# Optimization experiments

Hardware: AMD Instinct MI355X
Metric: run time of the kernel (lower is better)

Reference implementation:

```python
import jax, jax.numpy as jnp
import numpy as np

B, D, T, H = 1024, 128, 256, 64  # batch, input_dim, seq_len, hidden_dim


def _lstm_layer(x_proj, w_hh):
    """x_proj: [B, T, 4H] precomputed input projection (incl. both biases).
    Returns (all hidden states [B, T, H], final hidden [B, H])."""
    b = x_proj.shape[0]
    h0 = jnp.zeros((b, H), x_proj.dtype)
    c0 = jnp.zeros((b, H), x_proj.dtype)

    def step(carry, xt):
        h, c = carry
        gates = xt + h @ w_hh.T  # [B, 4H]; PyTorch gate order i, f, g, o
        i, f, g, o = jnp.split(gates, 4, axis=-1)
        i = jax.nn.sigmoid(i)
        f = jax.nn.sigmoid(f)
        g = jnp.tanh(g)
        o = jax.nn.sigmoid(o)
        c = f * c + i * g
        h = o * jnp.tanh(c)
        return (h, c), h

    (hT, _), ys = jax.lax.scan(step, (h0, c0), x_proj.transpose(1, 0, 2))
    return ys.transpose(1, 0, 2), hT


def setup_inputs() -> dict:
    key = jax.random.key(0)
    ks = jax.random.split(key, 11)
    s = 1.0 / np.sqrt(H)  # PyTorch LSTM init scale
    return {
        "x": jax.random.normal(ks[0], (B, D, T), jnp.float32),
        "w_ih0": jax.random.normal(ks[1], (4 * H, D), jnp.float32) * s,
        "w_hh0": jax.random.normal(ks[2], (4 * H, H), jnp.float32) * s,
        "b_ih0": jax.random.normal(ks[3], (4 * H,), jnp.float32) * s,
        "b_hh0": jax.random.normal(ks[4], (4 * H,), jnp.float32) * s,
        "w_ih1": jax.random.normal(ks[5], (4 * H, H), jnp.float32) * s,
        "w_hh1": jax.random.normal(ks[6], (4 * H, H), jnp.float32) * s,
        "b_ih1": jax.random.normal(ks[7], (4 * H,), jnp.float32) * s,
        "b_hh1": jax.random.normal(ks[8], (4 * H,), jnp.float32) * s,
        "w_fc": jax.random.normal(ks[9], (D, H), jnp.float32) * s,
        "b_fc": jax.random.normal(ks[10], (D,), jnp.float32) * s,
    }


def reference(x, w_ih0, w_hh0, b_ih0, b_hh0, w_ih1, w_hh1, b_ih1, b_hh1, w_fc, b_fc):
    # x: [B, input_dim, T] -> permute(0, 2, 1) -> [B, T, input_dim]
    xt = x.transpose(0, 2, 1)
    # Layer 0: precompute input projection for all timesteps (one big GEMM)
    xp0 = xt @ w_ih0.T + (b_ih0 + b_hh0)  # [B, T, 4H]
    ys0, _ = _lstm_layer(xp0, w_hh0)
    # Inter-layer dropout(p=0.3) is identity in eval/inference mode.
    xp1 = ys0 @ w_ih1.T + (b_ih1 + b_hh1)  # [B, T, 4H]
    _, hT = _lstm_layer(xp1, w_hh1)
    # Final-timestep linear head: lstm_out[:, -1, :] == final hidden state hT
    scores = hT @ w_fc.T + b_fc  # [B, input_dim]
    return scores
```

## Files before the change

### kernel.cpp

```cpp
#include <hip/hip_runtime.h>

#define PH  72
#define HSZ 1152
#define XRW 144
#define XSL 584

typedef float f32x4 __attribute__((ext_vector_type(4)));
typedef _Float16 f16x8 __attribute__((ext_vector_type(8)));

__device__ __forceinline__ float sigmoid_f(float x) {
    float e = __builtin_amdgcn_exp2f(-1.4426950408889634f * x);
    return __builtin_amdgcn_rcpf(1.0f + e);
}
__device__ __forceinline__ float tanh_f(float x) {
    float e = __builtin_amdgcn_exp2f(-2.8853900817779268f * x);
    return 2.0f * __builtin_amdgcn_rcpf(1.0f + e) - 1.0f;
}
__device__ __forceinline__ f16x8 load_frag16h(const float* wp, int n, int K, int k0) {
    const float* wf = wp + (size_t)n * K + k0;
    f16x8 h;
    #pragma unroll
    for (int j = 0; j < 8; ++j) h[j] = (_Float16)wf[j];
    return h;
}
__device__ __forceinline__ void load_frag16(const float* wp, int n, int K, int k0,
                                            f16x8& hi, f16x8& lo) {
    const float* wf = wp + (size_t)n * K + k0;
    #pragma unroll
    for (int j = 0; j < 8; ++j) {
        const float v = wf[j];
        const _Float16 h = (_Float16)v;
        hi[j] = h;
        lo[j] = (_Float16)(v - (float)h);
    }
}
__device__ __forceinline__ void gload16(const void* g, void* l) {
    __builtin_amdgcn_global_load_lds(
        (const __attribute__((address_space(1))) unsigned int*)g,
        (__attribute__((address_space(3))) unsigned int*)l, 16, 0, 0);
}

#define MFMA16(a, b, c) __builtin_amdgcn_mfma_f32_16x16x32_f16(a, b, c, 0, 0, 0)

__global__ __launch_bounds__(768, 3) void rec_fused(
    const float* __restrict__ x,
    const float* __restrict__ wih0, const float* __restrict__ whh0,
    const float* __restrict__ bih0, const float* __restrict__ bhh0,
    const float* __restrict__ wih1, const float* __restrict__ whh1,
    const float* __restrict__ bih1, const float* __restrict__ bhh1,
    const float* __restrict__ wfc,  const float* __restrict__ bfc,
    float* __restrict__ out)
{
    __shared__ float    xs32[4 * 2048];
    __shared__ _Float16 xh[32 * XSL];
    __shared__ float    xpl[4 * 1024];
    __shared__ _Float16 h0[2 * HSZ], h1[2 * HSZ];
    const int tid = threadIdx.x, lane = tid & 63, w = tid >> 6;
    const int l16 = lane & 15, quad = lane >> 4, k0 = quad * 8;
    const int wl = w & 3;
    const int role = w >> 2;
    const bool is1 = (role == 0), is0 = (role == 1), isP = (role == 2);
    const int bb  = blockIdx.x & 63;
    const int sub = blockIdx.x >> 6;

    const float* xrow = x + (size_t)(bb * 16 + wl * 4 + sub) * 128 * 256;

    f16x8 fA[4][2], fB[4][4];
    float gb[4] = {0.f, 0.f, 0.f, 0.f};
    #pragma unroll
    for (int g = 0; g < 4; ++g) {
        const int n = g * 64 + wl * 16 + l16;
        if (is1) {
            #pragma unroll
            for (int ks = 0; ks < 2; ++ks) {
                fA[g][ks] = load_frag16h(wih1, n, 64, ks * 32 + k0);
                load_frag16(whh1, n, 64, ks * 32 + k0, fB[g][ks], fB[g][2 + ks]);
            }
            gb[g] = bih1[n] + bhh1[n];
        } else if (is0) {
            #pragma unroll
            for (int ks = 0; ks < 2; ++ks)
                load_frag16(whh0, n, 64, ks * 32 + k0, fA[g][ks], fB[g][2 + ks]);
        } else {
            #pragma unroll
            for (int ks = 0; ks < 4; ++ks)
                fB[g][ks] = load_frag16h(wih0, n, 128, ks * 32 + k0);
            gb[g] = bih0[n] + bhh0[n];
        }
    }
    for (int i = tid; i < 2 * HSZ; i += 768) { h0[i] = (_Float16)0.f; h1[i] = (_Float16)0.f; }
    float c = 0.f;

    auto convert_rows = [&](int cc, int ib0, int nib) {
        const int sb = (cc & 1) * 16;
        const int tq = lane & 3;
        for (int ib = ib0; ib < ib0 + nib; ++ib) {
            const float4 v = *(const float4*)&xs32[wl * 2048 + ib * 256 + lane * 4];
            const int d = ib * 16 + (lane >> 2);
            const float vv[4] = {v.x, v.y, v.z, v.w};
            #pragma unroll
            for (int j = 0; j < 4; ++j)
                xh[(sb + tq * 4 + j) * XSL + wl * XRW + d] = (_Float16)vv[j];
        }
    };
    auto issue_chunk = [&](int cc) {
        #pragma unroll
        for (int ib = 0; ib < 8; ++ib)
            gload16(xrow + (size_t)(ib * 16 + (lane >> 2)) * 256 + cc * 16 + (lane & 3) * 4,
                    (char*)xs32 + wl * 8192 + ib * 1024);
    };
    auto compute_xp = [&](int tp) {
        const int fs = ((tp >> 4) & 1) * 16 + (tp & 15);
        f16x8 ax[4];
        #pragma unroll
        for (int ks = 0; ks < 4; ++ks)
            ax[ks] = *(const f16x8*)&xh[fs * XSL + (l16 >> 2) * XRW + ks * 32 + k0];
        f32x4 pa[4];
        #pragma unroll
        for (int g = 0; g < 4; ++g) pa[g] = (f32x4){gb[g], 0.f, 0.f, 0.f};
        #pragma unroll
        for (int g = 0; g < 4; ++g)
            #pragma unroll
            for (int ks = 0; ks < 4; ++ks)
                pa[g] = MFMA16(ax[ks], fB[g][ks], pa[g]);
        f32x4 o;
        o[0] = pa[0][0]; o[1] = pa[1][0]; o[2] = pa[2][0]; o[3] = pa[3][0];
        *(f32x4*)&xpl[(((tp & 3) * 4 + wl) * 64 + lane) * 4] = o;
    };

    if (isP) issue_chunk(0);
    __syncthreads();
    if (isP) { convert_rows(0, 0, 8); issue_chunk(1); }
    __syncthreads();
    if (isP) { compute_xp(0); compute_xp(1); }
    __syncthreads();
    if (is0) {
        const f32x4 xp4 = *(const f32x4*)&xpl[(wl * 64 + lane) * 4];
        const float gi = sigmoid_f(xp4[0]);
        const float gg = tanh_f(xp4[2]);
        const float go = sigmoid_f(xp4[3]);
        c = gi * gg;
        h0[(quad * 4) * PH + wl * 16 + l16] = (_Float16)(go * tanh_f(c));
    }
    __syncthreads();

    for (int t = 0; t < 255; ++t) {
        const int s0 = t & 1, s1 = s0 ^ 1;
        const int tn = t + 1;
        if (is1) {
            f16x8 ah[2], bh[2];
            #pragma unroll
            for (int ks = 0; ks < 2; ++ks) {
                ah[ks] = *(const f16x8*)&h0[s0 * HSZ + l16 * PH + ks * 32 + k0];
                bh[ks] = *(const f16x8*)&h1[s1 * HSZ + l16 * PH + ks * 32 + k0];
            }
            f32x4 accA[4], accB[4];
            #pragma unroll
            for (int g = 0; g < 4; ++g) {
                accA[g] = (f32x4){gb[g], 0.f, 0.f, 0.f};
                accB[g] = (f32x4){0.f, 0.f, 0.f, 0.f};
            }
            #pragma unroll
            for (int g = 0; g < 4; ++g)
                #pragma unroll
                for (int ks = 0; ks < 2; ++ks) {
                    accA[g] = MFMA16(ah[ks], fA[g][ks], accA[g]);
                    accA[g] = MFMA16(bh[ks], fB[g][ks], accA[g]);
                    accB[g] = MFMA16(bh[ks], fB[g][2 + ks], accB[g]);
                }
            const float gi = sigmoid_f(accA[0][0] + accB[0][0]);
            const float gf = sigmoid_f(accA[1][0] + accB[1][0]);
            const float gg = tanh_f(accA[2][0] + accB[2][0]);
            const float go = sigmoid_f(accA[3][0] + accB[3][0]);
            c = gf * c + gi * gg;
            h1[s0 * HSZ + (quad * 4) * PH + wl * 16 + l16] =
                (_Float16)(go * tanh_f(c));
        } else if (is0) {
            const f32x4 xp4 =
                *(const f32x4*)&xpl[(((tn & 3) * 4 + wl) * 64 + lane) * 4];
            f16x8 ah[2];
            #pragma unroll
            for (int ks = 0; ks < 2; ++ks)
                ah[ks] = *(const f16x8*)&h0[s0 * HSZ + l16 * PH + ks * 32 + k0];
            f32x4 accA[4], accB[4];
            #pragma unroll
            for (int g = 0; g < 4; ++g) {
                accA[g] = (f32x4){xp4[g], 0.f, 0.f, 0.f};
                accB[g] = (f32x4){0.f, 0.f, 0.f, 0.f};
            }
            #pragma unroll
            for (int g = 0; g < 4; ++g)
                #pragma unroll
                for (int ks = 0; ks < 2; ++ks) {
                    accA[g] = MFMA16(ah[ks], fA[g][ks], accA[g]);
                    accB[g] = MFMA16(ah[ks], fB[g][2 + ks], accB[g]);
                }
            const float gi = sigmoid_f(accA[0][0] + accB[0][0]);
            const float gf = sigmoid_f(accA[1][0] + accB[1][0]);
            const float gg = tanh_f(accA[2][0] + accB[2][0]);
            const float go = sigmoid_f(accA[3][0] + accB[3][0]);
            c = gf * c + gi * gg;
            h0[s1 * HSZ + (quad * 4) * PH + wl * 16 + l16] =
                (_Float16)(go * tanh_f(c));
        } else {
            if ((tn & 15) == 0 && tn < 240)
                issue_chunk((tn >> 4) + 1);
            const int m16 = tn & 15;
            if (m16 >= 8 && m16 < 12 && tn < 248)
                convert_rows((tn >> 4) + 1, (m16 - 8) * 2, 2);
            const int tp = t + 2;
            if (tp <= 255) compute_xp(tp);
        }
        __syncthreads();
    }

    if (is1) {
        f16x8 ah[2], bh[2];
        #pragma unroll
        for (int ks = 0; ks < 2; ++ks) {
            ah[ks] = *(const f16x8*)&h0[HSZ + l16 * PH + ks * 32 + k0];
            bh[ks] = *(const f16x8*)&h1[l16 * PH + ks * 32 + k0];
        }
        f32x4 accA[4], accB[4];
        #pragma unroll
        for (int g = 0; g < 4; ++g) {
            accA[g] = (f32x4){gb[g], 0.f, 0.f, 0.f};
            accB[g] = (f32x4){0.f, 0.f, 0.f, 0.f};
        }
        #pragma unroll
        for (int g = 0; g < 4; ++g)
            #pragma unroll
            for (int ks = 0; ks < 2; ++ks) {
                accA[g] = MFMA16(ah[ks], fA[g][ks], accA[g]);
                accA[g] = MFMA16(bh[ks], fB[g][ks], accA[g]);
                accB[g] = MFMA16(bh[ks], fB[g][2 + ks], accB[g]);
            }
        const float gi = sigmoid_f(accA[0][0] + accB[0][0]);
        const float gf = sigmoid_f(accA[1][0] + accB[1][0]);
        const float gg = tanh_f(accA[2][0] + accB[2][0]);
        const float go = sigmoid_f(accA[3][0] + accB[3][0]);
        c = gf * c + gi * gg;
        h1[HSZ + (quad * 4) * PH + wl * 16 + l16] = (_Float16)(go * tanh_f(c));
    }
    __syncthreads();

    if (tid < 512) {
        const int n   = tid & 127;
        const int sel = tid >> 7;
        float s = 0.f;
        for (int k = 0; k < 64; ++k)
            s += (float)h1[HSZ + (sel * 4) * PH + k] * wfc[n * 64 + k];
        out[(size_t)(bb * 16 + sel * 4 + sub) * 128 + n] = s + bfc[n];
    }
}

extern "C" void kernel_launch(void* const* d_in, const int* in_sizes, int n_in,
                              void* d_out, int out_size, void* d_ws, size_t ws_size,
                              hipStream_t stream) {
    const float* x     = (const float*)d_in[0];
    const float* wih0  = (const float*)d_in[1];
    const float* whh0  = (const float*)d_in[2];
    const float* bih0  = (const float*)d_in[3];
    const float* bhh0  = (const float*)d_in[4];
    const float* wih1  = (const float*)d_in[5];
    const float* whh1  = (const float*)d_in[6];
    const float* bih1  = (const float*)d_in[7];
    const float* bhh1  = (const float*)d_in[8];
    const float* wfc   = (const float*)d_in[9];
    const float* bfc   = (const float*)d_in[10];
    float* out = (float*)d_out;

    rec_fused<<<256, 768, 0, stream>>>(x, wih0, whh0, bih0, bhh0,
                                       wih1, whh1, bih1, bhh1, wfc, bfc, out);
}
```

Measured before the change: 365.8 us.

## Prefetch projection inputs into registers and prioritize recurrent waves

The layer-0 waves now load their input-projection vector one step ahead into a register. The projection waves preload their x fragments from LDS a step early and compute the projection three timesteps ahead instead of two. The recurrent waves raise their scheduling priority with s_setprio during the gate math. The goal is to take LDS load latency off the serial per-step critical path and let the recurrent waves win issue slots over the projection work, at the cost of extra live registers and a deeper ring of buffer slots.

```diff
diff --git a/kernel.cpp b/kernel.cpp
--- a/kernel.cpp
+++ b/kernel.cpp
@@ -90,6 +90,8 @@
     }
     for (int i = tid; i < 2 * HSZ; i += 768) { h0[i] = (_Float16)0.f; h1[i] = (_Float16)0.f; }
     float c = 0.f;
+    f32x4 xpr;
+    f16x8 axr[4];
 
     auto convert_rows = [&](int cc, int ib0, int nib) {
         const int sb = (cc & 1) * 16;
@@ -132,15 +134,21 @@
     __syncthreads();
     if (isP) { convert_rows(0, 0, 8); issue_chunk(1); }
     __syncthreads();
-    if (isP) { compute_xp(0); compute_xp(1); }
+    if (isP) { compute_xp(0); compute_xp(1); compute_xp(2); }
     __syncthreads();
     if (is0) {
-        const f32x4 xp4 = *(const f32x4*)&xpl[(wl * 64 + lane) * 4];
-        const float gi = sigmoid_f(xp4[0]);
-        const float gg = tanh_f(xp4[2]);
-        const float go = sigmoid_f(xp4[3]);
+        xpr = *(const f32x4*)&xpl[(wl * 64 + lane) * 4];
+        const float gi = sigmoid_f(xpr[0]);
+        const float gg = tanh_f(xpr[2]);
+        const float go = sigmoid_f(xpr[3]);
         c = gi * gg;
         h0[(quad * 4) * PH + wl * 16 + l16] = (_Float16)(go * tanh_f(c));
+        xpr = *(const f32x4*)&xpl[((1 * 4 + wl) * 64 + lane) * 4];
+    }
+    if (isP) {
+        #pragma unroll
+        for (int ks = 0; ks < 4; ++ks)
+            axr[ks] = *(const f16x8*)&xh[3 * XSL + (l16 >> 2) * XRW + ks * 32 + k0];
     }
     __syncthreads();
 
@@ -148,6 +156,7 @@
         const int s0 = t & 1, s1 = s0 ^ 1;
         const int tn = t + 1;
         if (is1) {
+            __builtin_amdgcn_s_setprio(1);
             f16x8 ah[2], bh[2];
             #pragma unroll
             for (int ks = 0; ks < 2; ++ks) {
@@ -175,9 +184,9 @@
             c = gf * c + gi * gg;
             h1[s0 * HSZ + (quad * 4) * PH + wl * 16 + l16] =
                 (_Float16)(go * tanh_f(c));
+            __builtin_amdgcn_s_setprio(0);
         } else if (is0) {
-            const f32x4 xp4 =
-                *(const f32x4*)&xpl[(((tn & 3) * 4 + wl) * 64 + lane) * 4];
+            __builtin_amdgcn_s_setprio(1);
             f16x8 ah[2];
             #pragma unroll
             for (int ks = 0; ks < 2; ++ks)
@@ -185,7 +194,7 @@
             f32x4 accA[4], accB[4];
             #pragma unroll
             for (int g = 0; g < 4; ++g) {
-                accA[g] = (f32x4){xp4[g], 0.f, 0.f, 0.f};
+                accA[g] = (f32x4){xpr[g], 0.f, 0.f, 0.f};
                 accB[g] = (f32x4){0.f, 0.f, 0.f, 0.f};
             }
             #pragma unroll
@@ -202,14 +211,38 @@
             c = gf * c + gi * gg;
             h0[s1 * HSZ + (quad * 4) * PH + wl * 16 + l16] =
                 (_Float16)(go * tanh_f(c));
+            __builtin_amdgcn_s_setprio(0);
+            if (tn < 255) {
+                const int tq = tn + 1;
+                xpr = *(const f32x4*)&xpl[(((tq & 3) * 4 + wl) * 64 + lane) * 4];
+            }
         } else {
+            const int tp = t + 3;
+            if (tp <= 255) {
+                f32x4 pa[4];
+                #pragma unroll
+                for (int g = 0; g < 4; ++g) pa[g] = (f32x4){gb[g], 0.f, 0.f, 0.f};
+                #pragma unroll
+                for (int g = 0; g < 4; ++g)
+                    #pragma unroll
+                    for (int ks = 0; ks < 4; ++ks)
+                        pa[g] = MFMA16(axr[ks], fB[g][ks], pa[g]);
+                f32x4 o;
+                o[0] = pa[0][0]; o[1] = pa[1][0]; o[2] = pa[2][0]; o[3] = pa[3][0];
+                *(f32x4*)&xpl[(((tp & 3) * 4 + wl) * 64 + lane) * 4] = o;
+            }
             if ((tn & 15) == 0 && tn < 240)
                 issue_chunk((tn >> 4) + 1);
             const int m16 = tn & 15;
             if (m16 >= 8 && m16 < 12 && tn < 248)
                 convert_rows((tn >> 4) + 1, (m16 - 8) * 2, 2);
-            const int tp = t + 2;
-            if (tp <= 255) compute_xp(tp);
+            const int tpn = t + 4;
+            if (tpn <= 255) {
+                const int fs = ((tpn >> 4) & 1) * 16 + (tpn & 15);
+                #pragma unroll
+                for (int ks = 0; ks < 4; ++ks)
+                    axr[ks] = *(const f16x8*)&xh[fs * XSL + (l16 >> 2) * XRW + ks * 32 + k0];
+            }
         }
         __syncthreads();
     }
```

Result: slower. 525.7 us (+43.7%).

## Move fp16 hi/lo split from recurrent weights to hidden state rows

Applied to the files above, without the earlier changes.

Recurrent weights are now held as a single fp16 fragment, and the fp16 residual error is carried in the hidden state instead. Each h is stored as a hi value plus a lo residual in the next M-row, so one MFMA per gate/k-step yields hi and lo contributions in separate output rows that are summed. This removes one MFMA chain and the second accumulator per gate in the critical recurrence. The input-projection pipeline is also deepened by one step, with compute_xp issued before chunk loads. The weight rounding error is no longer compensated, which costs some accuracy.

```diff
diff --git a/kernel.cpp b/kernel.cpp
--- a/kernel.cpp
+++ b/kernel.cpp
@@ -22,17 +22,6 @@
     #pragma unroll
     for (int j = 0; j < 8; ++j) h[j] = (_Float16)wf[j];
     return h;
-}
-__device__ __forceinline__ void load_frag16(const float* wp, int n, int K, int k0,
-                                            f16x8& hi, f16x8& lo) {
-    const float* wf = wp + (size_t)n * K + k0;
-    #pragma unroll
-    for (int j = 0; j < 8; ++j) {
-        const float v = wf[j];
-        const _Float16 h = (_Float16)v;
-        hi[j] = h;
-        lo[j] = (_Float16)(v - (float)h);
-    }
 }
 __device__ __forceinline__ void gload16(const void* g, void* l) {
     __builtin_amdgcn_global_load_lds(
@@ -74,13 +63,13 @@
             #pragma unroll
             for (int ks = 0; ks < 2; ++ks) {
                 fA[g][ks] = load_frag16h(wih1, n, 64, ks * 32 + k0);
-                load_frag16(whh1, n, 64, ks * 32 + k0, fB[g][ks], fB[g][2 + ks]);
+                fB[g][ks] = load_frag16h(whh1, n, 64, ks * 32 + k0);
             }
             gb[g] = bih1[n] + bhh1[n];
         } else if (is0) {
             #pragma unroll
             for (int ks = 0; ks < 2; ++ks)
-                load_frag16(whh0, n, 64, ks * 32 + k0, fA[g][ks], fB[g][2 + ks]);
+                fA[g][ks] = load_frag16h(whh0, n, 64, ks * 32 + k0);
         } else {
             #pragma unroll
             for (int ks = 0; ks < 4; ++ks)
@@ -127,12 +116,18 @@
         o[0] = pa[0][0]; o[1] = pa[1][0]; o[2] = pa[2][0]; o[3] = pa[3][0];
         *(f32x4*)&xpl[(((tp & 3) * 4 + wl) * 64 + lane) * 4] = o;
     };
+    auto store_h = [&](_Float16* hbuf, int slot, float hv) {
+        const _Float16 hh = (_Float16)hv;
+        const int base = slot * HSZ + (quad * 4) * PH + wl * 16 + l16;
+        hbuf[base]      = hh;
+        hbuf[base + PH] = (_Float16)(hv - (float)hh);
+    };
 
     if (isP) issue_chunk(0);
     __syncthreads();
     if (isP) { convert_rows(0, 0, 8); issue_chunk(1); }
     __syncthreads();
-    if (isP) { compute_xp(0); compute_xp(1); }
+    if (isP) { compute_xp(0); compute_xp(1); compute_xp(2); }
     __syncthreads();
     if (is0) {
         const f32x4 xp4 = *(const f32x4*)&xpl[(wl * 64 + lane) * 4];
@@ -140,7 +135,7 @@
         const float gg = tanh_f(xp4[2]);
         const float go = sigmoid_f(xp4[3]);
         c = gi * gg;
-        h0[(quad * 4) * PH + wl * 16 + l16] = (_Float16)(go * tanh_f(c));
+        store_h(h0, 0, go * tanh_f(c));
     }
     __syncthreads();
 
@@ -154,27 +149,23 @@
                 ah[ks] = *(const f16x8*)&h0[s0 * HSZ + l16 * PH + ks * 32 + k0];
                 bh[ks] = *(const f16x8*)&h1[s1 * HSZ + l16 * PH + ks * 32 + k0];
             }
-            f32x4 accA[4], accB[4];
-            #pragma unroll
-            for (int g = 0; g < 4; ++g) {
-                accA[g] = (f32x4){gb[g], 0.f, 0.f, 0.f};
-                accB[g] = (f32x4){0.f, 0.f, 0.f, 0.f};
-            }
+            f32x4 acc[4];
+            #pragma unroll
+            for (int g = 0; g < 4; ++g)
+                acc[g] = (f32x4){gb[g], 0.f, 0.f, 0.f};
             #pragma unroll
             for (int g = 0; g < 4; ++g)
                 #pragma unroll
                 for (int ks = 0; ks < 2; ++ks) {
-                    accA[g] = MFMA16(ah[ks], fA[g][ks], accA[g]);
-                    accA[g] = MFMA16(bh[ks], fB[g][ks], accA[g]);
-                    accB[g] = MFMA16(bh[ks], fB[g][2 + ks], accB[g]);
+                    acc[g] = MFMA16(ah[ks], fA[g][ks], acc[g]);
+                    acc[g] = MFMA16(bh[ks], fB[g][ks], acc[g]);
                 }
-            const float gi = sigmoid_f(accA[0][0] + accB[0][0]);
-            const float gf = sigmoid_f(accA[1][0] + accB[1][0]);
-            const float gg = tanh_f(accA[2][0] + accB[2][0]);
-            const float go = sigmoid_f(accA[3][0] + accB[3][0]);
+            const float gi = sigmoid_f(acc[0][0] + acc[0][1]);
+            const float gf = sigmoid_f(acc[1][0] + acc[1][1]);
+            const float gg = tanh_f(acc[2][0] + acc[2][1]);
+            const float go = sigmoid_f(acc[3][0] + acc[3][1]);
             c = gf * c + gi * gg;
-            h1[s0 * HSZ + (quad * 4) * PH + wl * 16 + l16] =
-                (_Float16)(go * tanh_f(c));
+            store_h(h1, s0, go * tanh_f(c));
         } else if (is0) {
             const f32x4 xp4 =
                 *(const f32x4*)&xpl[(((tn & 3) * 4 + wl) * 64 + lane) * 4];
@@ -182,34 +173,29 @@
             #pragma unroll
             for (int ks = 0; ks < 2; ++ks)
                 ah[ks] = *(const f16x8*)&h0[s0 * HSZ + l16 * PH + ks * 32 + k0];
-            f32x4 accA[4], accB[4];
-            #pragma unroll
-            for (int g = 0; g < 4; ++g) {
-                accA[g] = (f32x4){xp4[g], 0.f, 0.f, 0.f};
-                accB[g] = (f32x4){0.f, 0.f, 0.f, 0.f};
-            }
+            f32x4 acc[4];
+            #pragma unroll
+            for (int g = 0; g < 4; ++g)
+                acc[g] = (f32x4){xp4[g], 0.f, 0.f, 0.f};
             #pragma unroll
             for (int g = 0; g < 4; ++g)
                 #pragma unroll
-                for (int ks = 0; ks < 2; ++ks) {
-                    accA[g] = MFMA16(ah[ks], fA[g][ks], accA[g]);
-                    accB[g] = MFMA16(ah[ks], fB[g][2 + ks], accB[g]);
-                }
-            const float gi = sigmoid_f(accA[0][0] + accB[0][0]);
-            const float gf = sigmoid_f(accA[1][0] + accB[1][0]);
-            const float gg = tanh_f(accA[2][0] + accB[2][0]);
-            const float go = sigmoid_f(accA[3][0] + accB[3][0]);
+                for (int ks = 0; ks < 2; ++ks)
+                    acc[g] = MFMA16(ah[ks], fA[g][ks], acc[g]);
+            const float gi = sigmoid_f(acc[0][0] + acc[0][1]);
+            const float gf = sigmoid_f(acc[1][0] + acc[1][1]);
+            const float gg = tanh_f(acc[2][0] + acc[2][1]);
+            const float go = sigmoid_f(acc[3][0] + acc[3][1]);
             c = gf * c + gi * gg;
-            h0[s1 * HSZ + (quad * 4) * PH + wl * 16 + l16] =
-                (_Float16)(go * tanh_f(c));
+            store_h(h0, s1, go * tanh_f(c));
         } else {
+            const int tp = t + 3;
+            if (tp <= 255) compute_xp(tp);
             if ((tn & 15) == 0 && tn < 240)
                 issue_chunk((tn >> 4) + 1);
             const int m16 = tn & 15;
             if (m16 >= 8 && m16 < 12 && tn < 248)
                 convert_rows((tn >> 4) + 1, (m16 - 8) * 2, 2);
-            const int tp = t + 2;
-            if (tp <= 255) compute_xp(tp);
         }
         __syncthreads();
     }
@@ -221,26 +207,23 @@
             ah[ks] = *(const f16x8*)&h0[HSZ + l16 * PH + ks * 32 + k0];
             bh[ks] = *(const f16x8*)&h1[l16 * PH + ks * 32 + k0];
         }
-        f32x4 accA[4], accB[4];
-        #pragma unroll
-        for (int g = 0; g < 4; ++g) {
-            accA[g] = (f32x4){gb[g], 0.f, 0.f, 0.f};
-            accB[g] = (f32x4){0.f, 0.f, 0.f, 0.f};
-        }
+        f32x4 acc[4];
         #pragma unroll
         for (int g = 0; g < 4; ++g)
+            acc[g] = (f32x4){gb[g], 0.f, 0.f, 0.f};
+        #pragma unroll
+        for (int g = 0; g < 4; ++g)
             #pragma unroll
             for (int ks = 0; ks < 2; ++ks) {
-                accA[g] = MFMA16(ah[ks], fA[g][ks], accA[g]);
-                accA[g] = MFMA16(bh[ks], fB[g][ks], accA[g]);
-                accB[g] = MFMA16(bh[ks], fB[g][2 + ks], accB[g]);
+                acc[g] = MFMA16(ah[ks], fA[g][ks], acc[g]);
+                acc[g] = MFMA16(bh[ks], fB[g][ks], acc[g]);
             }
-        const float gi = sigmoid_f(accA[0][0] + accB[0][0]);
-        const float gf = sigmoid_f(accA[1][0] + accB[1][0]);
-        const float gg = tanh_f(accA[2][0] + accB[2][0]);
-        const float go = sigmoid_f(accA[3][0] + accB[3][0]);
+        const float gi = sigmoid_f(acc[0][0] + acc[0][1]);
+        const float gf = sigmoid_f(acc[1][0] + acc[1][1]);
+        const float gg = tanh_f(acc[2][0] + acc[2][1]);
+        const float go = sigmoid_f(acc[3][0] + acc[3][1]);
         c = gf * c + gi * gg;
-        h1[HSZ + (quad * 4) * PH + wl * 16 + l16] = (_Float16)(go * tanh_f(c));
+        store_h(h1, 1, go * tanh_f(c));
     }
     __syncthreads();
 
@@ -249,7 +232,8 @@
         const int sel = tid >> 7;
         float s = 0.f;
         for (int k = 0; k < 64; ++k)
-            s += (float)h1[HSZ + (sel * 4) * PH + k] * wfc[n * 64 + k];
+            s += ((float)h1[HSZ + (sel * 4) * PH + k]
+                + (float)h1[HSZ + (sel * 4 + 1) * PH + k]) * wfc[n * 64 + k];
         out[(size_t)(bb * 16 + sel * 4 + sub) * 128 + n] = s + bfc[n];
     }
 }
```

Measured after the change: 348.8 us. 4.7% less time.
